# Performance work log

Measured on AMD Instinct MI355X. Metric: run time of the kernel, lower is better.

Reference implementation:

```python
import jax, jax.numpy as jnp
import numpy as np

N_NODES = 50000
N_EDGES = 1600000
L_BACK = 168
L_FORE = 24
H = 256
THETA_B = 167  # 2*int(168/2-1)+1
THETA_F = 23   # 2*int(24/2-1)+1
EPS = 1e-5


def make_basis(L):
    h = L // 2 - 1  # int(L/2 - 1)
    t = np.arange(L, dtype=np.float64) / L * 2.0 * np.pi
    rows = [np.ones(L)] + [np.cos(t * i) for i in range(1, h + 1)] + [np.sin(t * i) for i in range(1, h + 1)]
    return jnp.asarray(np.stack(rows, axis=0), dtype=jnp.float32)  # [2h+1, L]


def batch_norm(x, gamma, beta):
    # training-mode BatchNorm1d: biased variance over the node axis
    m = jnp.mean(x, axis=0)
    v = jnp.mean((x - m) ** 2, axis=0)
    return (x - m) * jax.lax.rsqrt(v + EPS) * gamma + beta


def gcn_conv(x, W, b, src, dst, n):
    # PyG GCNConv with self-loops, symmetric normalization, edge_weight=None
    xw = x @ W  # [N, H]
    deg = jnp.zeros((n,), dtype=x.dtype).at[dst].add(1.0)  # self-loops included in src/dst
    dinv = jax.lax.rsqrt(deg)
    norm = dinv[src] * dinv[dst]  # [E+N]
    msg = xw[src] * norm[:, None]
    out = jnp.zeros_like(xw).at[dst].add(msg)
    return out + b


def setup_inputs() -> dict:
    key = jax.random.key(0)
    ks = jax.random.split(key, 16)
    d = {}
    d['x'] = jax.random.normal(ks[0], (N_NODES, L_BACK), dtype=jnp.float32)
    d['edge_index'] = jax.random.randint(ks[1], (2, N_EDGES), 0, N_NODES, dtype=jnp.int32)
    s = 0.02
    # MLP stack (Linear weights stored as [in, out])
    d['w1'] = jax.random.normal(ks[2], (L_BACK, H), jnp.float32) * s
    d['b1'] = jnp.zeros((H,), jnp.float32)
    d['g1'] = jnp.ones((H,), jnp.float32)
    d['bt1'] = jnp.zeros((H,), jnp.float32)
    d['w2'] = jax.random.normal(ks[3], (H, H), jnp.float32) * s
    d['b2'] = jnp.zeros((H,), jnp.float32)
    d['g2'] = jnp.ones((H,), jnp.float32)
    d['bt2'] = jnp.zeros((H,), jnp.float32)
    # GCN stack (2 layers)
    d['gw1'] = jax.random.normal(ks[4], (H, H), jnp.float32) * s
    d['gb1'] = jnp.zeros((H,), jnp.float32)
    d['gg1'] = jnp.ones((H,), jnp.float32)
    d['gbt1'] = jnp.zeros((H,), jnp.float32)
    d['gw2'] = jax.random.normal(ks[5], (H, H), jnp.float32) * s
    d['gb2'] = jnp.zeros((H,), jnp.float32)
    d['gg2'] = jnp.ones((H,), jnp.float32)
    d['gbt2'] = jnp.zeros((H,), jnp.float32)
    # theta projections (no bias)
    d['tbW'] = jax.random.normal(ks[6], (H, THETA_B), jnp.float32) * s
    d['tfW'] = jax.random.normal(ks[7], (H, THETA_F), jnp.float32) * s
    # fixed Fourier bases
    d['basis_b'] = make_basis(L_BACK)  # [167, 168]
    d['basis_f'] = make_basis(L_FORE)  # [23, 24]
    return d


def reference(x, edge_index, w1, b1, g1, bt1, w2, b2, g2, bt2,
              gw1, gb1, gg1, gbt1, gw2, gb2, gg2, gbt2,
              tbW, tfW, basis_b, basis_f):
    n = x.shape[0]
    # add self-loops once
    loop = jnp.arange(n, dtype=edge_index.dtype)
    src = jnp.concatenate([edge_index[0], loop])
    dst = jnp.concatenate([edge_index[1], loop])
    # MLP stack: Linear -> ReLU -> BN (dropout is identity in eval)
    h = batch_norm(jax.nn.relu(x @ w1 + b1), g1, bt1)
    h = batch_norm(jax.nn.relu(h @ w2 + b2), g2, bt2)
    # GCN stack: GCNConv -> ReLU -> BN
    h = batch_norm(jax.nn.relu(gcn_conv(h, gw1, gb1, src, dst, n)), gg1, gbt1)
    h = batch_norm(jax.nn.relu(gcn_conv(h, gw2, gb2, src, dst, n)), gg2, gbt2)
    backcast = (h @ tbW) @ basis_b  # [N, 168]
    forecast = (h @ tfW) @ basis_f  # [N, 24]
    return backcast, forecast
```

## Files before the change

kernel.cpp:

```cpp
#include <hip/hip_runtime.h>
#include <stdint.h>

#define NNODES 50000
#define NEDGES 1600000
#define HD 256
#define EPSV 1e-5f
#define CAP 80

typedef unsigned short u16;
typedef __attribute__((ext_vector_type(8))) short short8;
typedef __attribute__((ext_vector_type(4))) float f32x4;

__device__ __forceinline__ u16 f2b(float f) {
  union { float f; uint32_t u; } c; c.f = f;
  uint32_t u = c.u;
  u += 0x7fffu + ((u >> 16) & 1u);
  return (u16)(u >> 16);
}
__device__ __forceinline__ float b2f(u16 s) {
  union { uint32_t u; float f; } c; c.u = ((uint32_t)s) << 16;
  return c.f;
}

__device__ __forceinline__ void gl2lds16(const u16* g, u16* l) {
  __builtin_amdgcn_global_load_lds(
      (__attribute__((address_space(1))) void*)(void*)g,
      (__attribute__((address_space(3))) void*)(void*)l, 16, 0, 0);
}

__global__ void setup_k(int* __restrict__ cur, u16* __restrict__ csr, float* __restrict__ st,
                        const float* __restrict__ w1, u16* __restrict__ W1T,
                        const float* __restrict__ tbW, const float* __restrict__ tfW,
                        const float* __restrict__ bb, const float* __restrict__ bf,
                        float* __restrict__ Mc) {
  int b = blockIdx.x, t = threadIdx.x;
  if (b < 196) {
    int i = b * 256 + t;
    if (i < NNODES) { cur[i] = 1; csr[(size_t)i * CAP] = (u16)i; }
    if (i < 4 * 8 * 512) st[i] = 0.f;
  } else if (b < 452) {
    int n = b - 196;
    if (t < 192) W1T[n * 192 + t] = (t < 168) ? f2b(w1[t * HD + n]) : (u16)0;
  } else {
    int k = b - 452;
    if (t < 192) {
      float s = 0.f;
      if (t < 168) {
        for (int i = 0; i < 167; ++i) s += tbW[k * 167 + i] * bb[i * 168 + t];
      } else {
        int n2 = t - 168;
        for (int i = 0; i < 23; ++i) s += tfW[k * 23 + i] * bf[i * 24 + n2];
      }
      Mc[k * 192 + t] = s;
    }
  }
}

template <int NT, int NCB, bool AF32, bool RELU, bool SPLIT, bool DSCALE, bool STATS, bool FILL>
__global__ __launch_bounds__(256) void gemm_k(const void* __restrict__ Ap, int M, int Kpad,
                                              int lda, int Klim,
                                              const u16* __restrict__ WT,
                                              const float* __restrict__ extra,
                                              const int* __restrict__ curp,
                                              void* __restrict__ outp, float* __restrict__ out2,
                                              float* __restrict__ stout,
                                              const int* __restrict__ esrc,
                                              const int* __restrict__ edst,
                                              int* __restrict__ fcur, u16* __restrict__ fcsr,
                                              int eoff, int eend) {
  constexpr int BROWS = NT * 16;
  const int bid = (int)blockIdx.x;
  if constexpr (FILL) {
    int gemmblks = ((M + 63) / 64) * NCB;
    int fb = bid - gemmblks;
    if (fb >= 0) {
      int e = eoff + fb * 256 + (int)threadIdx.x;
      if (e < eend) {
        int d = edst[e];
        int p = atomicAdd(&fcur[d], 1);
        if (p < CAP) fcsr[(size_t)d * CAP + p] = (u16)esrc[e];
      }
      return;
    }
  }
  __shared__ __align__(16) u16 Alds[2][64][32];
  __shared__ __align__(16) u16 Blds[2][BROWS][32];
  constexpr int SR = STATS ? 4 : 1;
  constexpr int SC = STATS ? BROWS : 1;
  __shared__ float sred[SR][SC];
  __shared__ float qred[SR][SC];
  const int tid = threadIdx.x;
  const int wave = tid >> 6, lane = tid & 63;
  const int quad = lane >> 4, l16 = lane & 15;
  const int cb = bid % NCB;
  const int row0 = (bid / NCB) * 64;
  const int col0 = cb * BROWS;

  f32x4 acc[NT];
#pragma unroll
  for (int i = 0; i < NT; ++i) acc[i] = (f32x4){0.f, 0.f, 0.f, 0.f};

  const int am = tid >> 2;
  const int akc = (tid & 3) * 8;
  const int arow = row0 + am;

  for (int k0 = 0; k0 < Kpad; k0 += 64) {
    if constexpr (AF32) {
      const float* A = (const float*)Ap;
#pragma unroll
      for (int p = 0; p < 2; ++p) {
        uint4 pack = {0u, 0u, 0u, 0u};
        int kk = k0 + p * 32 + akc;
        if (arow < M && kk < Klim) {
          const float* pp = A + (size_t)arow * lda + kk;
          float4 fa = *(const float4*)pp;
          float4 fb = *(const float4*)(pp + 4);
          pack.x = (uint32_t)f2b(fa.x) | ((uint32_t)f2b(fa.y) << 16);
          pack.y = (uint32_t)f2b(fa.z) | ((uint32_t)f2b(fa.w) << 16);
          pack.z = (uint32_t)f2b(fb.x) | ((uint32_t)f2b(fb.y) << 16);
          pack.w = (uint32_t)f2b(fb.z) | ((uint32_t)f2b(fb.w) << 16);
        }
        *(uint4*)(&Alds[p][0][0] + (size_t)tid * 8) = pack;
      }
    } else {
      const u16* A = (const u16*)Ap;
      if (arow < M) {
        gl2lds16(A + (size_t)arow * lda + k0 + akc, &Alds[0][0][0] + (size_t)tid * 8);
        gl2lds16(A + (size_t)arow * lda + k0 + 32 + akc, &Alds[1][0][0] + (size_t)tid * 8);
      }
    }
#pragma unroll
    for (int p = 0; p < 2; ++p) {
#pragma unroll
      for (int j = 0; j < (BROWS + 63) / 64; ++j) {
        int br = j * 64 + am;
        if (br < BROWS)
          gl2lds16(WT + (size_t)(col0 + br) * Kpad + k0 + p * 32 + akc,
                   &Blds[p][0][0] + (size_t)j * 2048 + (size_t)tid * 8);
      }
    }
    __syncthreads();
    short8 av0 = *(const short8*)&Alds[0][wave * 16 + l16][quad * 8];
    short8 av1 = *(const short8*)&Alds[1][wave * 16 + l16][quad * 8];
#pragma unroll
    for (int nt = 0; nt < NT; ++nt) {
      short8 bv0 = *(const short8*)&Blds[0][nt * 16 + l16][quad * 8];
      short8 bv1 = *(const short8*)&Blds[1][nt * 16 + l16][quad * 8];
      acc[nt] = __builtin_amdgcn_mfma_f32_16x16x32_bf16(av0, bv0, acc[nt], 0, 0, 0);
      acc[nt] = __builtin_amdgcn_mfma_f32_16x16x32_bf16(av1, bv1, acc[nt], 0, 0, 0);
    }
    __syncthreads();
  }

#pragma unroll
  for (int nt = 0; nt < NT; ++nt) {
    float s = 0.f, q = 0.f;
    int col = col0 + nt * 16 + l16;
#pragma unroll
    for (int r = 0; r < 4; ++r) {
      int row = row0 + wave * 16 + quad * 4 + r;
      if (row >= M) continue;
      float v = acc[nt][r] + extra[col];
      if constexpr (RELU) v = fmaxf(v, 0.f);
      if constexpr (DSCALE) v *= rsqrtf((float)curp[row]);
      if constexpr (SPLIT) {
        if (col < 168) ((float*)outp)[(size_t)row * 168 + col] = v;
        else ((float*)out2)[(size_t)row * 24 + (col - 168)] = v;
      } else {
        ((u16*)outp)[(size_t)row * HD + col] = f2b(v);
      }
      if constexpr (STATS) { s += v; q += v * v; }
    }
    if constexpr (STATS) {
      s += __shfl_xor(s, 16); s += __shfl_xor(s, 32);
      q += __shfl_xor(q, 16); q += __shfl_xor(q, 32);
      if (quad == 0) { sred[wave][nt * 16 + l16] = s; qred[wave][nt * 16 + l16] = q; }
    }
  }
  if constexpr (STATS) {
    __syncthreads();
    if (tid < BROWS) {
      float s = sred[0][tid] + sred[1][tid] + sred[2][tid] + sred[3][tid];
      float q = qred[0][tid] + qred[1][tid] + qred[2][tid] + qred[3][tid];
      int sl = (bid & 7) * 512;
      atomicAdd(&stout[sl + col0 + tid], s);
      atomicAdd(&stout[sl + 256 + col0 + tid], q);
    }
  }
}

__global__ __launch_bounds__(256) void fold_k(const float* __restrict__ st, float invM,
                                              const float* __restrict__ gamma,
                                              const float* __restrict__ beta,
                                              const float* __restrict__ W, int ncols,
                                              const float* __restrict__ bias,
                                              u16* __restrict__ WT, float* __restrict__ extra) {
  int n = blockIdx.x, k = threadIdx.x;
  float sm = 0.f, sq = 0.f;
#pragma unroll
  for (int s = 0; s < 8; ++s) { sm += st[s * 512 + k]; sq += st[s * 512 + 256 + k]; }
  float m = sm * invM;
  float v = sq * invM - m * m;
  float sc = gamma[k] * rsqrtf(v + EPSV);
  float sh = beta[k] - m * sc;
  float w = W[(size_t)k * ncols + n];
  WT[(size_t)n * HD + k] = f2b(sc * w);
  __shared__ float red[256];
  red[k] = sh * w;
  __syncthreads();
  for (int d = 128; d > 0; d >>= 1) {
    if (k < d) red[k] += red[k + d];
    __syncthreads();
  }
  if (k == 0) extra[n] = (bias ? bias[n] : 0.f) + red[0];
}

__global__ __launch_bounds__(256) void agg_k(const u16* __restrict__ csr,
                                             const int* __restrict__ deg,
                                             const u16* __restrict__ xw,
                                             const float* __restrict__ gb, u16* __restrict__ out,
                                             float* __restrict__ stout) {
  __shared__ float ss[4][256];
  __shared__ float qq[4][256];
  int wave = threadIdx.x >> 6, lane = threadIdx.x & 63;
  int dst = blockIdx.x * 4 + wave;
  bool valid = dst < NNODES;
  const int c = lane * 4;
  float r0 = 0.f, r1 = 0.f, r2 = 0.f, r3 = 0.f;
  if (valid) {
    int dv = min(deg[dst], CAP);
    int p0 = dst * CAP;
    int p1 = p0 + dv;
    float a0 = 0.f, a1 = 0.f, a2 = 0.f, a3 = 0.f;
    int p = p0;
#define ACCUM(vv)                              \
  a0 += b2f((u16)((vv).x & 0xffffu));          \
  a1 += b2f((u16)((vv).x >> 16));              \
  a2 += b2f((u16)((vv).y & 0xffffu));          \
  a3 += b2f((u16)((vv).y >> 16));
    for (; p + 8 <= p1; p += 8) {
      uint4 sw = *(const uint4*)&csr[p];
      int s0 = sw.x & 0xffff, s1 = sw.x >> 16;
      int s2 = sw.y & 0xffff, s3 = sw.y >> 16;
      int s4 = sw.z & 0xffff, s5 = sw.z >> 16;
      int s6 = sw.w & 0xffff, s7 = sw.w >> 16;
      uint2 v0 = *(const uint2*)&xw[(size_t)s0 * HD + c];
      uint2 v1 = *(const uint2*)&xw[(size_t)s1 * HD + c];
      uint2 v2 = *(const uint2*)&xw[(size_t)s2 * HD + c];
      uint2 v3 = *(const uint2*)&xw[(size_t)s3 * HD + c];
      uint2 v4 = *(const uint2*)&xw[(size_t)s4 * HD + c];
      uint2 v5 = *(const uint2*)&xw[(size_t)s5 * HD + c];
      uint2 v6 = *(const uint2*)&xw[(size_t)s6 * HD + c];
      uint2 v7 = *(const uint2*)&xw[(size_t)s7 * HD + c];
      ACCUM(v0); ACCUM(v1); ACCUM(v2); ACCUM(v3);
      ACCUM(v4); ACCUM(v5); ACCUM(v6); ACCUM(v7);
    }
    for (; p < p1; ++p) {
      int s = csr[p];
      uint2 v = *(const uint2*)&xw[(size_t)s * HD + c];
      ACCUM(v);
    }
#undef ACCUM
    float dd = rsqrtf((float)dv);
    float4 gv = *(const float4*)&gb[c];
    r0 = fmaxf(dd * a0 + gv.x, 0.f);
    r1 = fmaxf(dd * a1 + gv.y, 0.f);
    r2 = fmaxf(dd * a2 + gv.z, 0.f);
    r3 = fmaxf(dd * a3 + gv.w, 0.f);
    uint2 o;
    o.x = (uint32_t)f2b(r0) | ((uint32_t)f2b(r1) << 16);
    o.y = (uint32_t)f2b(r2) | ((uint32_t)f2b(r3) << 16);
    *(uint2*)&out[(size_t)dst * HD + c] = o;
  }
  ss[wave][c + 0] = r0; ss[wave][c + 1] = r1; ss[wave][c + 2] = r2; ss[wave][c + 3] = r3;
  qq[wave][c + 0] = r0 * r0; qq[wave][c + 1] = r1 * r1;
  qq[wave][c + 2] = r2 * r2; qq[wave][c + 3] = r3 * r3;
  __syncthreads();
  int t = threadIdx.x;
  float s = ss[0][t] + ss[1][t] + ss[2][t] + ss[3][t];
  float q = qq[0][t] + qq[1][t] + qq[2][t] + qq[3][t];
  int sl = (blockIdx.x & 7) * 512;
  atomicAdd(&stout[sl + t], s);
  atomicAdd(&stout[sl + 256 + t], q);
}


extern "C" void kernel_launch(void* const* d_in, const int* in_sizes, int n_in,
                              void* d_out, int out_size, void* d_ws, size_t ws_size,
                              hipStream_t stream) {
  const float* x = (const float*)d_in[0];
  const int* ei = (const int*)d_in[1];
  const float* w1 = (const float*)d_in[2];
  const float* b1 = (const float*)d_in[3];
  const float* g1 = (const float*)d_in[4];
  const float* bt1 = (const float*)d_in[5];
  const float* w2 = (const float*)d_in[6];
  const float* b2 = (const float*)d_in[7];
  const float* g2 = (const float*)d_in[8];
  const float* bt2 = (const float*)d_in[9];
  const float* gw1 = (const float*)d_in[10];
  const float* gb1 = (const float*)d_in[11];
  const float* gg1 = (const float*)d_in[12];
  const float* gbt1 = (const float*)d_in[13];
  const float* gw2 = (const float*)d_in[14];
  const float* gb2 = (const float*)d_in[15];
  const float* gg2 = (const float*)d_in[16];
  const float* gbt2 = (const float*)d_in[17];
  const float* tbW = (const float*)d_in[18];
  const float* tfW = (const float*)d_in[19];
  const float* bb = (const float*)d_in[20];
  const float* bfb = (const float*)d_in[21];
  const int* esrc = ei;
  const int* edst = ei + NEDGES;

  char* wsp = (char*)d_ws;
  size_t off = 0;
  auto alloc = [&](size_t b) {
    void* p = wsp + off;
    off += (b + 511) & ~(size_t)511;
    return p;
  };
  u16* buf1 = (u16*)alloc((size_t)NNODES * HD * 2);
  u16* buf2 = (u16*)alloc((size_t)NNODES * HD * 2);
  u16* csr = (u16*)alloc((size_t)NNODES * CAP * 2);
  int* cur = (int*)alloc((size_t)NNODES * 4);
  float* st = (float*)alloc((size_t)4 * 8 * 512 * 4);
  u16* W1T = (u16*)alloc(256 * 192 * 2);
  u16* WT = (u16*)alloc(256 * 256 * 2);
  float* Mc = (float*)alloc(256 * 192 * 4);
  float* extra = (float*)alloc(256 * 4);

  float* backc = (float*)d_out;
  float* forec = backc + (size_t)NNODES * 168;
  const float invM = 1.0f / (float)NNODES;

  const int GB = (NNODES + 63) / 64;
  const int HALF = NEDGES / 2;
  const int FB = HALF / 256;

  setup_k<<<708, 256, 0, stream>>>(cur, csr, st, w1, W1T, tbW, tfW, bb, bfb, Mc);

  gemm_k<8, 2, true, true, false, false, true, true><<<GB * 2 + FB, 256, 0, stream>>>(
      x, NNODES, 192, 168, 168, W1T, b1, nullptr, buf1, nullptr, st,
      esrc, edst, cur, csr, 0, HALF);
  fold_k<<<256, 256, 0, stream>>>(st, invM, g1, bt1, w2, 256, b2, WT, extra);
  gemm_k<8, 2, false, true, false, false, true, true><<<GB * 2 + FB, 256, 0, stream>>>(
      buf1, NNODES, 256, 256, 256, WT, extra, nullptr, buf2, nullptr, st + 4096,
      esrc, edst, cur, csr, HALF, NEDGES);
  fold_k<<<256, 256, 0, stream>>>(st + 4096, invM, g2, bt2, gw1, 256, nullptr, WT, extra);
  gemm_k<8, 2, false, false, false, true, false, false><<<GB * 2, 256, 0, stream>>>(
      buf2, NNODES, 256, 256, 256, WT, extra, cur, buf1, nullptr, nullptr,
      nullptr, nullptr, nullptr, nullptr, 0, 0);
  agg_k<<<12500, 256, 0, stream>>>(csr, cur, buf1, gb1, buf2, st + 8192);
  fold_k<<<256, 256, 0, stream>>>(st + 8192, invM, gg1, gbt1, gw2, 256, nullptr, WT, extra);
  gemm_k<8, 2, false, false, false, true, false, false><<<GB * 2, 256, 0, stream>>>(
      buf2, NNODES, 256, 256, 256, WT, extra, cur, buf1, nullptr, nullptr,
      nullptr, nullptr, nullptr, nullptr, 0, 0);
  agg_k<<<12500, 256, 0, stream>>>(csr, cur, buf1, gb2, buf2, st + 12288);
  fold_k<<<192, 256, 0, stream>>>(st + 12288, invM, gg2, gbt2, Mc, 192, nullptr, WT, extra);
  gemm_k<6, 2, false, false, true, false, false, false><<<GB * 2, 256, 0, stream>>>(
      buf2, NNODES, 256, 256, 256, WT, extra, nullptr, backc, forec, nullptr,
      nullptr, nullptr, nullptr, nullptr, 0, 0);
}
```

Baseline: 591.7 us.

## Split CSR build across three GEMMs and move source-degree scaling into aggregation

The edge-bucketing work that builds the CSR was split in halves across the first two GEMM launches. It is now split into thirds, with the third GEMM (the first GCN projection) also taking a share. That GEMM can no longer scale rows by the source degree, because degrees are not final while it runs. So the first aggregation kernel now loads deg[src] per edge and applies rsqrt itself. This spreads the edge scatter work more evenly across the GEMM launches, at the cost of extra per-edge degree gathers in the first aggregation.

```diff
diff --git a/kernel.cpp b/kernel.cpp
--- a/kernel.cpp
+++ b/kernel.cpp
@@ -215,6 +215,7 @@
   if (k == 0) extra[n] = (bias ? bias[n] : 0.f) + red[0];
 }
 
+template <bool SRCSCALE>
 __global__ __launch_bounds__(256) void agg_k(const u16* __restrict__ csr,
                                              const int* __restrict__ deg,
                                              const u16* __restrict__ xw,
@@ -233,17 +234,25 @@
     int p1 = p0 + dv;
     float a0 = 0.f, a1 = 0.f, a2 = 0.f, a3 = 0.f;
     int p = p0;
-#define ACCUM(vv)                              \
-  a0 += b2f((u16)((vv).x & 0xffffu));          \
-  a1 += b2f((u16)((vv).x >> 16));              \
-  a2 += b2f((u16)((vv).y & 0xffffu));          \
-  a3 += b2f((u16)((vv).y >> 16));
+#define ACCUMS(vv, dd)                               \
+  a0 += (dd) * b2f((u16)((vv).x & 0xffffu));         \
+  a1 += (dd) * b2f((u16)((vv).x >> 16));             \
+  a2 += (dd) * b2f((u16)((vv).y & 0xffffu));         \
+  a3 += (dd) * b2f((u16)((vv).y >> 16));
     for (; p + 8 <= p1; p += 8) {
       uint4 sw = *(const uint4*)&csr[p];
       int s0 = sw.x & 0xffff, s1 = sw.x >> 16;
       int s2 = sw.y & 0xffff, s3 = sw.y >> 16;
       int s4 = sw.z & 0xffff, s5 = sw.z >> 16;
       int s6 = sw.w & 0xffff, s7 = sw.w >> 16;
+      float d0 = 1.f, d1 = 1.f, d2 = 1.f, d3 = 1.f;
+      float d4 = 1.f, d5 = 1.f, d6 = 1.f, d7 = 1.f;
+      if constexpr (SRCSCALE) {
+        d0 = rsqrtf((float)deg[s0]); d1 = rsqrtf((float)deg[s1]);
+        d2 = rsqrtf((float)deg[s2]); d3 = rsqrtf((float)deg[s3]);
+        d4 = rsqrtf((float)deg[s4]); d5 = rsqrtf((float)deg[s5]);
+        d6 = rsqrtf((float)deg[s6]); d7 = rsqrtf((float)deg[s7]);
+      }
       uint2 v0 = *(const uint2*)&xw[(size_t)s0 * HD + c];
       uint2 v1 = *(const uint2*)&xw[(size_t)s1 * HD + c];
       uint2 v2 = *(const uint2*)&xw[(size_t)s2 * HD + c];
@@ -252,15 +261,17 @@
       uint2 v5 = *(const uint2*)&xw[(size_t)s5 * HD + c];
       uint2 v6 = *(const uint2*)&xw[(size_t)s6 * HD + c];
       uint2 v7 = *(const uint2*)&xw[(size_t)s7 * HD + c];
-      ACCUM(v0); ACCUM(v1); ACCUM(v2); ACCUM(v3);
-      ACCUM(v4); ACCUM(v5); ACCUM(v6); ACCUM(v7);
+      ACCUMS(v0, d0); ACCUMS(v1, d1); ACCUMS(v2, d2); ACCUMS(v3, d3);
+      ACCUMS(v4, d4); ACCUMS(v5, d5); ACCUMS(v6, d6); ACCUMS(v7, d7);
     }
     for (; p < p1; ++p) {
       int s = csr[p];
+      float dd = 1.f;
+      if constexpr (SRCSCALE) dd = rsqrtf((float)deg[s]);
       uint2 v = *(const uint2*)&xw[(size_t)s * HD + c];
-      ACCUM(v);
-    }
-#undef ACCUM
+      ACCUMS(v, dd);
+    }
+#undef ACCUMS
     float dd = rsqrtf((float)dv);
     float4 gv = *(const float4*)&gb[c];
     r0 = fmaxf(dd * a0 + gv.x, 0.f);
@@ -335,28 +346,29 @@
   const float invM = 1.0f / (float)NNODES;
 
   const int GB = (NNODES + 63) / 64;
-  const int HALF = NEDGES / 2;
-  const int FB = HALF / 256;
+  const int FB3 = 2084;
+  const int T1 = 533376;
+  const int T2 = 1066752;
 
   setup_k<<<708, 256, 0, stream>>>(cur, csr, st, w1, W1T, tbW, tfW, bb, bfb, Mc);
 
-  gemm_k<8, 2, true, true, false, false, true, true><<<GB * 2 + FB, 256, 0, stream>>>(
+  gemm_k<8, 2, true, true, false, false, true, true><<<GB * 2 + FB3, 256, 0, stream>>>(
       x, NNODES, 192, 168, 168, W1T, b1, nullptr, buf1, nullptr, st,
-      esrc, edst, cur, csr, 0, HALF);
+      esrc, edst, cur, csr, 0, T1);
   fold_k<<<256, 256, 0, stream>>>(st, invM, g1, bt1, w2, 256, b2, WT, extra);
-  gemm_k<8, 2, false, true, false, false, true, true><<<GB * 2 + FB, 256, 0, stream>>>(
+  gemm_k<8, 2, false, true, false, false, true, true><<<GB * 2 + FB3, 256, 0, stream>>>(
       buf1, NNODES, 256, 256, 256, WT, extra, nullptr, buf2, nullptr, st + 4096,
-      esrc, edst, cur, csr, HALF, NEDGES);
+      esrc, edst, cur, csr, T1, T2);
   fold_k<<<256, 256, 0, stream>>>(st + 4096, invM, g2, bt2, gw1, 256, nullptr, WT, extra);
-  gemm_k<8, 2, false, false, false, true, false, false><<<GB * 2, 256, 0, stream>>>(
-      buf2, NNODES, 256, 256, 256, WT, extra, cur, buf1, nullptr, nullptr,
-      nullptr, nullptr, nullptr, nullptr, 0, 0);
-  agg_k<<<12500, 256, 0, stream>>>(csr, cur, buf1, gb1, buf2, st + 8192);
+  gemm_k<8, 2, false, false, false, false, false, true><<<GB * 2 + FB3, 256, 0, stream>>>(
+      buf2, NNODES, 256, 256, 256, WT, extra, nullptr, buf1, nullptr, nullptr,
+      esrc, edst, cur, csr, T2, NEDGES);
+  agg_k<true><<<12500, 256, 0, stream>>>(csr, cur, buf1, gb1, buf2, st + 8192);
   fold_k<<<256, 256, 0, stream>>>(st + 8192, invM, gg1, gbt1, gw2, 256, nullptr, WT, extra);
   gemm_k<8, 2, false, false, false, true, false, false><<<GB * 2, 256, 0, stream>>>(
       buf2, NNODES, 256, 256, 256, WT, extra, cur, buf1, nullptr, nullptr,
       nullptr, nullptr, nullptr, nullptr, 0, 0);
-  agg_k<<<12500, 256, 0, stream>>>(csr, cur, buf1, gb2, buf2, st + 12288);
+  agg_k<false><<<12500, 256, 0, stream>>>(csr, cur, buf1, gb2, buf2, st + 12288);
   fold_k<<<192, 256, 0, stream>>>(st + 12288, invM, gg2, gbt2, Mc, 192, nullptr, WT, extra);
   gemm_k<6, 2, false, false, true, false, false, false><<<GB * 2, 256, 0, stream>>>(
       buf2, NNODES, 256, 256, 256, WT, extra, nullptr, backc, forec, nullptr,
```

New measurement: 589.1 us, median of 2. Within noise of the previous version (-0.4%).
